# Performance work log

Hardware: AMD Instinct MI355X
Metric: run time of the kernel (lower is better)

## Reference

```python
import jax, jax.numpy as jnp
import numpy as np

B, S, D, H = 4, 4096, 1024, 16
DK = D // H  # 64


def setup_inputs() -> dict:
    key = jax.random.key(0)
    ks = jax.random.split(key, 8)
    scale = 1.0 / np.sqrt(D)
    return {
        "query": jax.random.normal(ks[0], (B, S, D), dtype=jnp.float32),
        "key": jax.random.normal(ks[1], (B, S, D), dtype=jnp.float32),
        "value": jax.random.normal(ks[2], (B, S, D), dtype=jnp.float32),
        "Wq": jax.random.normal(ks[3], (D, D), dtype=jnp.float32) * scale,
        "Wk": jax.random.normal(ks[4], (D, D), dtype=jnp.float32) * scale,
        "Wv": jax.random.normal(ks[5], (D, D), dtype=jnp.float32) * scale,
        "Wo": jax.random.normal(ks[6], (D, D), dtype=jnp.float32) * scale,
        "bo": jnp.zeros((D,), dtype=jnp.float32),
    }


def _phi(x):
    # ELU + 1 feature map
    return jax.nn.elu(x) + 1.0


def _heads(x, W):
    # torch Linear: y = x @ W.T; then [B,S,D] -> [B,H,S,DK]
    y = jnp.einsum("bsd,ed->bse", x, W)
    return y.reshape(x.shape[0], x.shape[1], H, DK).transpose(0, 2, 1, 3)


def reference(query, key, value, Wq, Wk, Wv, Wo, bo):
    Q = _phi(_heads(query, Wq))   # [B,H,Sq,DK]
    K = _phi(_heads(key, Wk))     # [B,H,Sk,DK]
    V = _heads(value, Wv)         # [B,H,Sk,DK]

    KV = jnp.einsum("bhsd,bhse->bhde", K, V)        # [B,H,DK,DK]
    num = jnp.einsum("bhqd,bhde->bhqe", Q, KV)       # [B,H,Sq,DK]
    den = jnp.einsum("bhqd,bhd->bhq", Q, K.sum(axis=2))  # [B,H,Sq]
    out = num / (den[..., None] + 1e-6)

    out = out.transpose(0, 2, 1, 3).reshape(query.shape[0], query.shape[1], D)
    return jnp.einsum("bsd,ed->bse", out, Wo) + bo
```

## Files before the change

kernel.cpp:

```cpp
#include <hip/hip_runtime.h>


typedef unsigned short ushort_t;
typedef __bf16 bf16x8 __attribute__((ext_vector_type(8)));
typedef float f32x4 __attribute__((ext_vector_type(4)));
typedef void gvoid_t __attribute__((address_space(1)));
typedef void svoid_t __attribute__((address_space(3)));

#define BB 4
#define SS 4096
#define DD 1024
#define HH 16
#define DKk 64
#define MM (BB * SS)

__device__ __forceinline__ ushort_t f2bf(float f) {
  unsigned int u = __float_as_uint(f);
  u += 0x7fffu + ((u >> 16) & 1u);
  return (ushort_t)(u >> 16);
}
__device__ __forceinline__ float b2f(ushort_t h) {
  return __uint_as_float(((unsigned int)h) << 16);
}
__device__ __forceinline__ void gld_lds16(const ushort_t* g, ushort_t* l) {
  __builtin_amdgcn_global_load_lds((gvoid_t*)g, (svoid_t*)l, 16, 0, 0);
}
__device__ __forceinline__ bf16x8 ldfrag(const ushort_t* p) {
  return *(const bf16x8*)p;
}

__global__ __launch_bounds__(256) void cast3_kernel(
    const float* __restrict__ q, const float* __restrict__ k, const float* __restrict__ v,
    ushort_t* __restrict__ qd, ushort_t* __restrict__ kd, ushort_t* __restrict__ vd) {
  const int z = blockIdx.y;
  const float* s = (z == 0) ? q : (z == 1) ? k : v;
  ushort_t* d = (z == 0) ? qd : (z == 1) ? kd : vd;
  size_t i = ((size_t)blockIdx.x * 256 + threadIdx.x) * 4;
  float4 f = *(const float4*)(s + i);
  ushort4 o;
  o.x = f2bf(f.x); o.y = f2bf(f.y); o.z = f2bf(f.z); o.w = f2bf(f.w);
  *(ushort4*)(d + i) = o;
}

__global__ __launch_bounds__(256) void cast4_kernel(
    const float* __restrict__ a, const float* __restrict__ b,
    const float* __restrict__ c, const float* __restrict__ e,
    ushort_t* __restrict__ ad, ushort_t* __restrict__ bd,
    ushort_t* __restrict__ cd, ushort_t* __restrict__ ed) {
  const int z = blockIdx.y;
  const float* s = (z == 0) ? a : (z == 1) ? b : (z == 2) ? c : e;
  ushort_t* d = (z == 0) ? ad : (z == 1) ? bd : (z == 2) ? cd : ed;
  size_t i = ((size_t)blockIdx.x * 256 + threadIdx.x) * 4;
  float4 f = *(const float4*)(s + i);
  ushort4 o;
  o.x = f2bf(f.x); o.y = f2bf(f.y); o.z = f2bf(f.z); o.w = f2bf(f.w);
  *(ushort4*)(d + i) = o;
}

__global__ __launch_bounds__(256) void proj_kernel(
    const ushort_t* __restrict__ qa, const ushort_t* __restrict__ ka, const ushort_t* __restrict__ va,
    const ushort_t* __restrict__ wq, const ushort_t* __restrict__ wk, const ushort_t* __restrict__ wv,
    ushort_t* __restrict__ Qp, ushort_t* __restrict__ Kp, ushort_t* __restrict__ Vp) {
  const int z = blockIdx.z;
  const ushort_t* A = (z == 0) ? qa : (z == 1) ? ka : va;
  const ushort_t* Bw = (z == 0) ? wq : (z == 1) ? wk : wv;
  ushort_t* Y = (z == 0) ? Qp : (z == 1) ? Kp : Vp;
  const bool act = (z < 2);

  __shared__ __align__(16) ushort_t Ash[2][128 * 32];
  __shared__ __align__(16) ushort_t Bsh[2][128 * 32];
  const int t = threadIdx.x;
  const int r_ = blockIdx.x, u_ = blockIdx.y;
  const int yb = r_ + 8 * (u_ & 7) + 64 * (u_ >> 6);
  const int xb = (u_ >> 3) & 7;
  const int m0 = yb * 128, n0 = xb * 128;
  const int w = t >> 6, lane = t & 63, q4 = lane >> 4, l16 = lane & 15;
  const int wm = (w >> 1) * 64, wn = (w & 1) * 64;
  const int srow = t >> 2, sch = (t & 3) * 8;

  f32x4 acc[4][4];
  const f32x4 zero = {0.f, 0.f, 0.f, 0.f};
#pragma unroll
  for (int i = 0; i < 4; i++)
#pragma unroll
    for (int j = 0; j < 4; j++) acc[i][j] = zero;

  const ushort_t* ga = A + (size_t)(m0 + srow) * 1024 + sch;
  const ushort_t* gb = Bw + (size_t)(n0 + srow) * 1024 + sch;

  gld_lds16(ga + 0, &Ash[0][t * 8]);
  gld_lds16(ga + 64 * 1024, &Ash[0][(256 + t) * 8]);
  gld_lds16(gb + 0, &Bsh[0][t * 8]);
  gld_lds16(gb + 64 * 1024, &Bsh[0][(256 + t) * 8]);
  __syncthreads();

  int cur = 0;
  for (int k0 = 0; k0 < 1024; k0 += 32, cur ^= 1) {
    if (k0 + 32 < 1024) {
      gld_lds16(ga + (k0 + 32), &Ash[cur ^ 1][t * 8]);
      gld_lds16(ga + (k0 + 32) + 64 * 1024, &Ash[cur ^ 1][(256 + t) * 8]);
      gld_lds16(gb + (k0 + 32), &Bsh[cur ^ 1][t * 8]);
      gld_lds16(gb + (k0 + 32) + 64 * 1024, &Bsh[cur ^ 1][(256 + t) * 8]);
    }
    bf16x8 af[4], bfm[4];
#pragma unroll
    for (int mi = 0; mi < 4; mi++) af[mi] = ldfrag(&Ash[cur][(wm + mi * 16 + l16) * 32 + q4 * 8]);
#pragma unroll
    for (int ni = 0; ni < 4; ni++) bfm[ni] = ldfrag(&Bsh[cur][(wn + ni * 16 + l16) * 32 + q4 * 8]);
#pragma unroll
    for (int mi = 0; mi < 4; mi++)
#pragma unroll
      for (int ni = 0; ni < 4; ni++)
        acc[mi][ni] = __builtin_amdgcn_mfma_f32_16x16x32_bf16(af[mi], bfm[ni], acc[mi][ni], 0, 0, 0);
    __syncthreads();
  }
#pragma unroll
  for (int mi = 0; mi < 4; mi++)
#pragma unroll
    for (int ni = 0; ni < 4; ni++) {
      int col = n0 + wn + ni * 16 + l16;
#pragma unroll
      for (int r = 0; r < 4; r++) {
        int row = m0 + wm + mi * 16 + q4 * 4 + r;
        float vv = acc[mi][ni][r];
        if (act) vv = (vv > 0.f) ? (vv + 1.f) : __expf(vv);
        Y[(size_t)row * 1024 + col] = f2bf(vv);
      }
    }
}

__global__ __launch_bounds__(256) void out_kernel(
    const ushort_t* __restrict__ A, const ushort_t* __restrict__ Bw,
    float* __restrict__ Of, const float* __restrict__ bias) {
  __shared__ __align__(16) ushort_t Ash[2][128 * 32];
  __shared__ __align__(16) ushort_t Bsh[2][128 * 32];
  const int t = threadIdx.x;
  const int r_ = blockIdx.x, u_ = blockIdx.y;
  const int yb = r_ + 8 * (u_ & 7) + 64 * (u_ >> 6);
  const int xb = (u_ >> 3) & 7;
  const int m0 = yb * 128, n0 = xb * 128;
  const int w = t >> 6, lane = t & 63, q4 = lane >> 4, l16 = lane & 15;
  const int wm = (w >> 1) * 64, wn = (w & 1) * 64;
  const int srow = t >> 2, sch = (t & 3) * 8;

  f32x4 acc[4][4];
  const f32x4 zero = {0.f, 0.f, 0.f, 0.f};
#pragma unroll
  for (int i = 0; i < 4; i++)
#pragma unroll
    for (int j = 0; j < 4; j++) acc[i][j] = zero;

  const ushort_t* ga = A + (size_t)(m0 + srow) * 1024 + sch;
  const ushort_t* gb = Bw + (size_t)(n0 + srow) * 1024 + sch;

  gld_lds16(ga + 0, &Ash[0][t * 8]);
  gld_lds16(ga + 64 * 1024, &Ash[0][(256 + t) * 8]);
  gld_lds16(gb + 0, &Bsh[0][t * 8]);
  gld_lds16(gb + 64 * 1024, &Bsh[0][(256 + t) * 8]);
  __syncthreads();

  int cur = 0;
  for (int k0 = 0; k0 < 1024; k0 += 32, cur ^= 1) {
    if (k0 + 32 < 1024) {
      gld_lds16(ga + (k0 + 32), &Ash[cur ^ 1][t * 8]);
      gld_lds16(ga + (k0 + 32) + 64 * 1024, &Ash[cur ^ 1][(256 + t) * 8]);
      gld_lds16(gb + (k0 + 32), &Bsh[cur ^ 1][t * 8]);
      gld_lds16(gb + (k0 + 32) + 64 * 1024, &Bsh[cur ^ 1][(256 + t) * 8]);
    }
    bf16x8 af[4], bfm[4];
#pragma unroll
    for (int mi = 0; mi < 4; mi++) af[mi] = ldfrag(&Ash[cur][(wm + mi * 16 + l16) * 32 + q4 * 8]);
#pragma unroll
    for (int ni = 0; ni < 4; ni++) bfm[ni] = ldfrag(&Bsh[cur][(wn + ni * 16 + l16) * 32 + q4 * 8]);
#pragma unroll
    for (int mi = 0; mi < 4; mi++)
#pragma unroll
      for (int ni = 0; ni < 4; ni++)
        acc[mi][ni] = __builtin_amdgcn_mfma_f32_16x16x32_bf16(af[mi], bfm[ni], acc[mi][ni], 0, 0, 0);
    __syncthreads();
  }
#pragma unroll
  for (int mi = 0; mi < 4; mi++)
#pragma unroll
    for (int ni = 0; ni < 4; ni++) {
      int col = n0 + wn + ni * 16 + l16;
      float bv = bias[col];
#pragma unroll
      for (int r = 0; r < 4; r++) {
        int row = m0 + wm + mi * 16 + q4 * 4 + r;
        Of[(size_t)row * 1024 + col] = acc[mi][ni][r] + bv;
      }
    }
}

__global__ __launch_bounds__(256) void kv_kernel(
    const ushort_t* __restrict__ Kp, const ushort_t* __restrict__ Vp,
    float* __restrict__ KVt, float* __restrict__ Ksum) {
  const int bh = blockIdx.y, b = bh >> 4, h = bh & 15;
  const int schunk = blockIdx.x * 256;
  const int t = threadIdx.x, w = t >> 6, lane = t & 63, q4 = lane >> 4, l16 = lane & 15;
  __shared__ ushort_t Ksh[64 * 66];
  __shared__ ushort_t Vsh[64 * 66];
  __shared__ float red[4][64];

  f32x4 acc[4];
  const f32x4 zero = {0.f, 0.f, 0.f, 0.f};
#pragma unroll
  for (int i = 0; i < 4; i++) acc[i] = zero;
  float ksum = 0.f;

  const int mat = t >> 7, tl = t & 127;
  const ushort_t* src = mat ? Vp : Kp;
  ushort_t* dsh = mat ? Vsh : Ksh;

  for (int tile = 0; tile < 4; tile++) {
    const int s0 = schunk + tile * 64;
#pragma unroll
    for (int i = 0; i < 4; i++) {
      int idx = i * 1024 + tl * 8;
      int r = idx >> 6, c = idx & 63;
      const ushort_t* g = src + (size_t)(b * 4096 + s0 + r) * 1024 + h * 64 + c;
      uint4 u = *(const uint4*)g;
      unsigned int* p = (unsigned int*)&dsh[r * 66 + c];
      p[0] = u.x; p[1] = u.y; p[2] = u.z; p[3] = u.w;
    }
    __syncthreads();
#pragma unroll
    for (int ks = 0; ks < 2; ks++) {
      ushort_t tb[8];
#pragma unroll
      for (int j = 0; j < 8; j++) tb[j] = Ksh[(ks * 32 + q4 * 8 + j) * 66 + w * 16 + l16];
      bf16x8 bfr; __builtin_memcpy(&bfr, tb, 16);
#pragma unroll
      for (int mi = 0; mi < 4; mi++) {
        ushort_t ta[8];
#pragma unroll
        for (int j = 0; j < 8; j++) ta[j] = Vsh[(ks * 32 + q4 * 8 + j) * 66 + mi * 16 + l16];
        bf16x8 afr; __builtin_memcpy(&afr, ta, 16);
        acc[mi] = __builtin_amdgcn_mfma_f32_16x16x32_bf16(afr, bfr, acc[mi], 0, 0, 0);
      }
    }
    {
      int d = t & 63;
#pragma unroll
      for (int r = 0; r < 16; r++) ksum += b2f(Ksh[((t >> 6) * 16 + r) * 66 + d]);
    }
    __syncthreads();
  }
#pragma unroll
  for (int mi = 0; mi < 4; mi++)
#pragma unroll
    for (int r = 0; r < 4; r++) {
      int e = mi * 16 + q4 * 4 + r, d = w * 16 + l16;
      atomicAdd(&KVt[(size_t)bh * 4096 + e * 64 + d], acc[mi][r]);
    }
  red[t >> 6][t & 63] = ksum;
  __syncthreads();
  if (t < 64) atomicAdd(&Ksum[bh * 64 + t], red[0][t] + red[1][t] + red[2][t] + red[3][t]);
}

__global__ __launch_bounds__(256) void num_kernel(
    const ushort_t* __restrict__ Qp, const float* __restrict__ KVt,
    const float* __restrict__ Ksum, ushort_t* __restrict__ Oc) {
  const int bh = blockIdx.y, b = bh >> 4, h = bh & 15;
  const int sblk = blockIdx.x * 256;
  const int t = threadIdx.x, w = t >> 6, lane = t & 63, q4 = lane >> 4, l16 = lane & 15;
  __shared__ __align__(16) ushort_t KVsh[64 * 72];
  __shared__ float Ks_sh[64];
  __shared__ float rden[256];

#pragma unroll
  for (int i = 0; i < 16; i++) {
    int idx = i * 256 + t;
    int e = idx >> 6, d = idx & 63;
    KVsh[e * 72 + d] = f2bf(KVt[(size_t)bh * 4096 + idx]);
  }
  if (t < 64) Ks_sh[t] = Ksum[bh * 64 + t];
  __syncthreads();

  {
    const ushort_t* qrow = Qp + (size_t)(b * 4096 + sblk + t) * 1024 + h * 64;
    float den = 1e-6f;
#pragma unroll
    for (int j = 0; j < 8; j++) {
      bf16x8 qv = ldfrag(qrow + j * 8);
#pragma unroll
      for (int e = 0; e < 8; e++) den += (float)qv[e] * Ks_sh[j * 8 + e];
    }
    rden[t] = 1.f / den;
  }
  __syncthreads();

  f32x4 acc[4][4];
  const f32x4 zero = {0.f, 0.f, 0.f, 0.f};
#pragma unroll
  for (int i = 0; i < 4; i++)
#pragma unroll
    for (int j = 0; j < 4; j++) acc[i][j] = zero;

#pragma unroll
  for (int ks = 0; ks < 2; ks++) {
    bf16x8 af[4], bfr[4];
#pragma unroll
    for (int mi = 0; mi < 4; mi++)
      af[mi] = ldfrag(Qp + (size_t)(b * 4096 + sblk + w * 64 + mi * 16 + l16) * 1024 + h * 64 + ks * 32 + q4 * 8);
#pragma unroll
    for (int ni = 0; ni < 4; ni++)
      bfr[ni] = ldfrag(&KVsh[(ni * 16 + l16) * 72 + ks * 32 + q4 * 8]);
#pragma unroll
    for (int mi = 0; mi < 4; mi++)
#pragma unroll
      for (int ni = 0; ni < 4; ni++)
        acc[mi][ni] = __builtin_amdgcn_mfma_f32_16x16x32_bf16(af[mi], bfr[ni], acc[mi][ni], 0, 0, 0);
  }
#pragma unroll
  for (int mi = 0; mi < 4; mi++)
#pragma unroll
    for (int ni = 0; ni < 4; ni++) {
      int e = ni * 16 + l16;
#pragma unroll
      for (int r = 0; r < 4; r++) {
        int srow = w * 64 + mi * 16 + q4 * 4 + r;
        float vv = acc[mi][ni][r] * rden[srow];
        Oc[(size_t)(b * 4096 + sblk + srow) * 1024 + h * 64 + e] = f2bf(vv);
      }
    }
}

extern "C" void kernel_launch(void* const* d_in, const int* in_sizes, int n_in,
                              void* d_out, int out_size, void* d_ws, size_t ws_size,
                              hipStream_t stream) {
  const float* q  = (const float*)d_in[0];
  const float* k  = (const float*)d_in[1];
  const float* v  = (const float*)d_in[2];
  const float* Wq = (const float*)d_in[3];
  const float* Wk = (const float*)d_in[4];
  const float* Wv = (const float*)d_in[5];
  const float* Wo = (const float*)d_in[6];
  const float* bo = (const float*)d_in[7];

  char* ws = (char*)d_ws;
  const size_t SZ_IN = (size_t)MM * DD * 2;
  ushort_t* qbf = (ushort_t*)(ws);
  ushort_t* kbf = (ushort_t*)(ws + SZ_IN);
  ushort_t* vbf = (ushort_t*)(ws + 2 * SZ_IN);
  ushort_t* wqb = (ushort_t*)(ws + 3 * SZ_IN);
  ushort_t* wkb = wqb + (size_t)1024 * 1024;
  ushort_t* wvb = wkb + (size_t)1024 * 1024;
  ushort_t* wob = wvb + (size_t)1024 * 1024;
  ushort_t* Qp  = (ushort_t*)(ws + 3 * SZ_IN + 4 * (size_t)2097152);
  ushort_t* Kp  = Qp + (size_t)MM * DD;
  ushort_t* Vp  = Kp + (size_t)MM * DD;
  float* KVt    = (float*)((char*)(Vp + (size_t)MM * DD));
  float* KsumP  = KVt + (size_t)64 * 4096;
  ushort_t* Oc  = qbf;
  float* outp   = (float*)d_out;

  hipMemsetAsync(KVt, 0, ((size_t)64 * 4096 + 64 * 64) * sizeof(float), stream);
  cast3_kernel<<<dim3(16384, 3), 256, 0, stream>>>(q, k, v, qbf, kbf, vbf);
  cast4_kernel<<<dim3(1024, 4), 256, 0, stream>>>(Wq, Wk, Wv, Wo, wqb, wkb, wvb, wob);
  proj_kernel<<<dim3(8, 128, 3), 256, 0, stream>>>(qbf, kbf, vbf, wqb, wkb, wvb, Qp, Kp, Vp);
  kv_kernel<<<dim3(16, 64), 256, 0, stream>>>(Kp, Vp, KVt, KsumP);
  num_kernel<<<dim3(16, 64), 256, 0, stream>>>(Qp, KVt, KsumP, Oc);
  out_kernel<<<dim3(8, 128), 256, 0, stream>>>(Oc, wob, outp, bo);
}
```

Measured before the change: 453.7 us.

## Replace 128x128 GEMMs with 256x256 tiled, swizzled, ping-pong scheduled GEMM core

Both the projection and output GEMMs now use a shared 256x256-tile core with 512 threads, BK=64, XOR-swizzled LDS layout, and a staged load schedule with explicit waitcnt, barriers and setprio around MFMA clusters. Blocks are remapped so consecutive blocks land on different XCDs. The larger tiles raise arithmetic intensity and cut global traffic, and the swizzle avoids LDS bank conflicts. In exchange, register and LDS pressure go up, and with 768 and 256 blocks the wave quantization could be worse.

After: 430.0 us. 5.2% less time.

```diff
diff --git a/kernel.cpp b/kernel.cpp
--- a/kernel.cpp
+++ b/kernel.cpp
@@ -13,6 +13,7 @@
 #define HH 16
 #define DKk 64
 #define MM (BB * SS)
+#define NKT 16
 
 __device__ __forceinline__ ushort_t f2bf(float f) {
   unsigned int u = __float_as_uint(f);
@@ -57,140 +58,181 @@
   *(ushort4*)(d + i) = o;
 }
 
-__global__ __launch_bounds__(256) void proj_kernel(
+__device__ __forceinline__ void gemm256_core(
+    const ushort_t* __restrict__ A, const ushort_t* __restrict__ Bw,
+    ushort_t* __restrict__ Ybf, float* __restrict__ Yf,
+    const float* __restrict__ bias, bool act, int m0, int n0) {
+  __shared__ __align__(16) ushort_t As[2][2][8192];
+  __shared__ __align__(16) ushort_t Bs[2][2][8192];
+  const int t = threadIdx.x;
+  const int w = t >> 6, lane = t & 63, q4 = lane >> 4, l16 = lane & 15;
+  const int wr = w >> 2, wc = w & 3;
+  const int srow = t >> 3;
+  const int scol = (((t & 7) ^ (srow & 7)) * 8);
+  const int swz = l16 & 7;
+
+  const ushort_t* gA = A + (size_t)(m0 + srow) * 1024 + scol;
+  const ushort_t* gB = Bw + (size_t)(n0 + srow) * 1024 + scol;
+
+  f32x4 acc[8][4];
+  const f32x4 zero = {0.f, 0.f, 0.f, 0.f};
+#pragma unroll
+  for (int i = 0; i < 8; ++i)
+#pragma unroll
+    for (int j = 0; j < 4; ++j) acc[i][j] = zero;
+
+  auto rdA = [&](int c, int mi, int kk) -> bf16x8 {
+    const int rowh = mi * 16 + l16;
+    const int slot = (kk * 4 + q4) ^ swz;
+    return ldfrag(&As[c][wr][rowh * 64 + slot * 8]);
+  };
+  auto rdB = [&](int c, int ni, int kk) -> bf16x8 {
+    const int rowh = (wc & 1) * 64 + ni * 16 + l16;
+    const int slot = (kk * 4 + q4) ^ swz;
+    return ldfrag(&Bs[c][wc >> 1][rowh * 64 + slot * 8]);
+  };
+  auto stageA = [&](int c, int h, int kt) {
+    const ushort_t* g = gA + (size_t)(h * 128) * 1024 + kt * 64;
+    gld_lds16(g, &As[c][h][t * 8]);
+    gld_lds16(g + 64 * 1024, &As[c][h][4096 + t * 8]);
+  };
+  auto stageB = [&](int c, int h, int kt) {
+    const ushort_t* g = gB + (size_t)(h * 128) * 1024 + kt * 64;
+    gld_lds16(g, &Bs[c][h][t * 8]);
+    gld_lds16(g + 64 * 1024, &Bs[c][h][4096 + t * 8]);
+  };
+
+  stageB(0, 0, 0); stageB(0, 1, 0);
+  stageA(0, 0, 0); stageA(0, 1, 0);
+  stageB(1, 0, 1); stageB(1, 1, 1);
+  asm volatile("s_waitcnt vmcnt(4)" ::: "memory");
+  __builtin_amdgcn_s_barrier();
+
+  bf16x8 aR[4][2], b0[2][2], b1[2][2];
+#pragma unroll 2
+  for (int kt = 0; kt < NKT; ++kt) {
+    const int c = kt & 1;
+#pragma unroll
+    for (int mi = 0; mi < 4; ++mi) { aR[mi][0] = rdA(c, mi, 0); aR[mi][1] = rdA(c, mi, 1); }
+#pragma unroll
+    for (int ni = 0; ni < 2; ++ni) { b0[ni][0] = rdB(c, ni, 0); b0[ni][1] = rdB(c, ni, 1); }
+    if (kt + 1 < NKT) stageA(c ^ 1, 0, kt + 1);
+    __builtin_amdgcn_s_barrier();
+    asm volatile("s_waitcnt lgkmcnt(0)" ::: "memory");
+    __builtin_amdgcn_sched_barrier(0);
+    __builtin_amdgcn_s_setprio(1);
+#pragma unroll
+    for (int mi = 0; mi < 4; ++mi)
+#pragma unroll
+      for (int ni = 0; ni < 2; ++ni) {
+        acc[mi][ni] = __builtin_amdgcn_mfma_f32_16x16x32_bf16(aR[mi][0], b0[ni][0], acc[mi][ni], 0, 0, 0);
+        acc[mi][ni] = __builtin_amdgcn_mfma_f32_16x16x32_bf16(aR[mi][1], b0[ni][1], acc[mi][ni], 0, 0, 0);
+      }
+    __builtin_amdgcn_s_setprio(0);
+    __builtin_amdgcn_s_barrier();
+#pragma unroll
+    for (int ni = 0; ni < 2; ++ni) { b1[ni][0] = rdB(c, ni + 2, 0); b1[ni][1] = rdB(c, ni + 2, 1); }
+    if (kt + 1 < NKT) stageA(c ^ 1, 1, kt + 1);
+    __builtin_amdgcn_s_barrier();
+    asm volatile("s_waitcnt lgkmcnt(0)" ::: "memory");
+    __builtin_amdgcn_sched_barrier(0);
+    __builtin_amdgcn_s_setprio(1);
+#pragma unroll
+    for (int mi = 0; mi < 4; ++mi)
+#pragma unroll
+      for (int ni = 0; ni < 2; ++ni) {
+        acc[mi][ni + 2] = __builtin_amdgcn_mfma_f32_16x16x32_bf16(aR[mi][0], b1[ni][0], acc[mi][ni + 2], 0, 0, 0);
+        acc[mi][ni + 2] = __builtin_amdgcn_mfma_f32_16x16x32_bf16(aR[mi][1], b1[ni][1], acc[mi][ni + 2], 0, 0, 0);
+      }
+    __builtin_amdgcn_s_setprio(0);
+    __builtin_amdgcn_s_barrier();
+#pragma unroll
+    for (int mi = 0; mi < 4; ++mi) { aR[mi][0] = rdA(c, mi + 4, 0); aR[mi][1] = rdA(c, mi + 4, 1); }
+    if (kt + 2 < NKT) stageB(c, 0, kt + 2);
+    __builtin_amdgcn_s_barrier();
+    asm volatile("s_waitcnt lgkmcnt(0)" ::: "memory");
+    __builtin_amdgcn_sched_barrier(0);
+    __builtin_amdgcn_s_setprio(1);
+#pragma unroll
+    for (int mi = 0; mi < 4; ++mi)
+#pragma unroll
+      for (int ni = 0; ni < 2; ++ni) {
+        acc[mi + 4][ni] = __builtin_amdgcn_mfma_f32_16x16x32_bf16(aR[mi][0], b0[ni][0], acc[mi + 4][ni], 0, 0, 0);
+        acc[mi + 4][ni] = __builtin_amdgcn_mfma_f32_16x16x32_bf16(aR[mi][1], b0[ni][1], acc[mi + 4][ni], 0, 0, 0);
+      }
+    __builtin_amdgcn_s_setprio(0);
+    __builtin_amdgcn_s_barrier();
+    if (kt + 2 < NKT) stageB(c, 1, kt + 2);
+    __builtin_amdgcn_s_barrier();
+    __builtin_amdgcn_s_setprio(1);
+#pragma unroll
+    for (int mi = 0; mi < 4; ++mi)
+#pragma unroll
+      for (int ni = 0; ni < 2; ++ni) {
+        acc[mi + 4][ni + 2] = __builtin_amdgcn_mfma_f32_16x16x32_bf16(aR[mi][0], b1[ni][0], acc[mi + 4][ni + 2], 0, 0, 0);
+        acc[mi + 4][ni + 2] = __builtin_amdgcn_mfma_f32_16x16x32_bf16(aR[mi][1], b1[ni][1], acc[mi + 4][ni + 2], 0, 0, 0);
+      }
+    __builtin_amdgcn_s_setprio(0);
+    if (kt < NKT - 2) {
+      asm volatile("s_waitcnt vmcnt(4)" ::: "memory");
+    } else if (kt == NKT - 2) {
+      asm volatile("s_waitcnt vmcnt(0)" ::: "memory");
+    }
+    __builtin_amdgcn_s_barrier();
+  }
+
+  if (Yf) {
+#pragma unroll
+    for (int mi = 0; mi < 8; ++mi)
+#pragma unroll
+      for (int ni = 0; ni < 4; ++ni) {
+        const int col = n0 + wc * 64 + ni * 16 + l16;
+        const float bv = bias[col];
+#pragma unroll
+        for (int r = 0; r < 4; ++r) {
+          const int row = m0 + wr * 128 + mi * 16 + q4 * 4 + r;
+          Yf[(size_t)row * 1024 + col] = acc[mi][ni][r] + bv;
+        }
+      }
+  } else {
+#pragma unroll
+    for (int mi = 0; mi < 8; ++mi)
+#pragma unroll
+      for (int ni = 0; ni < 4; ++ni) {
+        const int col = n0 + wc * 64 + ni * 16 + l16;
+#pragma unroll
+        for (int r = 0; r < 4; ++r) {
+          const int row = m0 + wr * 128 + mi * 16 + q4 * 4 + r;
+          float vv = acc[mi][ni][r];
+          if (act) vv = (vv > 0.f) ? (vv + 1.f) : __expf(vv);
+          Ybf[(size_t)row * 1024 + col] = f2bf(vv);
+        }
+      }
+  }
+}
+
+__global__ __launch_bounds__(512, 2) void proj256_kernel(
     const ushort_t* __restrict__ qa, const ushort_t* __restrict__ ka, const ushort_t* __restrict__ va,
     const ushort_t* __restrict__ wq, const ushort_t* __restrict__ wk, const ushort_t* __restrict__ wv,
     ushort_t* __restrict__ Qp, ushort_t* __restrict__ Kp, ushort_t* __restrict__ Vp) {
-  const int z = blockIdx.z;
+  const int raw = blockIdx.x;
+  const int logical = (raw & 7) * 96 + (raw >> 3);
+  const int z = logical >> 8;
+  const int rem = logical & 255;
+  const int m0 = (rem >> 2) * 256, n0 = (rem & 3) * 256;
   const ushort_t* A = (z == 0) ? qa : (z == 1) ? ka : va;
   const ushort_t* Bw = (z == 0) ? wq : (z == 1) ? wk : wv;
   ushort_t* Y = (z == 0) ? Qp : (z == 1) ? Kp : Vp;
-  const bool act = (z < 2);
-
-  __shared__ __align__(16) ushort_t Ash[2][128 * 32];
-  __shared__ __align__(16) ushort_t Bsh[2][128 * 32];
-  const int t = threadIdx.x;
-  const int r_ = blockIdx.x, u_ = blockIdx.y;
-  const int yb = r_ + 8 * (u_ & 7) + 64 * (u_ >> 6);
-  const int xb = (u_ >> 3) & 7;
-  const int m0 = yb * 128, n0 = xb * 128;
-  const int w = t >> 6, lane = t & 63, q4 = lane >> 4, l16 = lane & 15;
-  const int wm = (w >> 1) * 64, wn = (w & 1) * 64;
-  const int srow = t >> 2, sch = (t & 3) * 8;
-
-  f32x4 acc[4][4];
-  const f32x4 zero = {0.f, 0.f, 0.f, 0.f};
-#pragma unroll
-  for (int i = 0; i < 4; i++)
-#pragma unroll
-    for (int j = 0; j < 4; j++) acc[i][j] = zero;
-
-  const ushort_t* ga = A + (size_t)(m0 + srow) * 1024 + sch;
-  const ushort_t* gb = Bw + (size_t)(n0 + srow) * 1024 + sch;
-
-  gld_lds16(ga + 0, &Ash[0][t * 8]);
-  gld_lds16(ga + 64 * 1024, &Ash[0][(256 + t) * 8]);
-  gld_lds16(gb + 0, &Bsh[0][t * 8]);
-  gld_lds16(gb + 64 * 1024, &Bsh[0][(256 + t) * 8]);
-  __syncthreads();
-
-  int cur = 0;
-  for (int k0 = 0; k0 < 1024; k0 += 32, cur ^= 1) {
-    if (k0 + 32 < 1024) {
-      gld_lds16(ga + (k0 + 32), &Ash[cur ^ 1][t * 8]);
-      gld_lds16(ga + (k0 + 32) + 64 * 1024, &Ash[cur ^ 1][(256 + t) * 8]);
-      gld_lds16(gb + (k0 + 32), &Bsh[cur ^ 1][t * 8]);
-      gld_lds16(gb + (k0 + 32) + 64 * 1024, &Bsh[cur ^ 1][(256 + t) * 8]);
-    }
-    bf16x8 af[4], bfm[4];
-#pragma unroll
-    for (int mi = 0; mi < 4; mi++) af[mi] = ldfrag(&Ash[cur][(wm + mi * 16 + l16) * 32 + q4 * 8]);
-#pragma unroll
-    for (int ni = 0; ni < 4; ni++) bfm[ni] = ldfrag(&Bsh[cur][(wn + ni * 16 + l16) * 32 + q4 * 8]);
-#pragma unroll
-    for (int mi = 0; mi < 4; mi++)
-#pragma unroll
-      for (int ni = 0; ni < 4; ni++)
-        acc[mi][ni] = __builtin_amdgcn_mfma_f32_16x16x32_bf16(af[mi], bfm[ni], acc[mi][ni], 0, 0, 0);
-    __syncthreads();
-  }
-#pragma unroll
-  for (int mi = 0; mi < 4; mi++)
-#pragma unroll
-    for (int ni = 0; ni < 4; ni++) {
-      int col = n0 + wn + ni * 16 + l16;
-#pragma unroll
-      for (int r = 0; r < 4; r++) {
-        int row = m0 + wm + mi * 16 + q4 * 4 + r;
-        float vv = acc[mi][ni][r];
-        if (act) vv = (vv > 0.f) ? (vv + 1.f) : __expf(vv);
-        Y[(size_t)row * 1024 + col] = f2bf(vv);
-      }
-    }
-}
-
-__global__ __launch_bounds__(256) void out_kernel(
+  gemm256_core(A, Bw, Y, nullptr, nullptr, z < 2, m0, n0);
+}
+
+__global__ __launch_bounds__(512, 2) void out256_kernel(
     const ushort_t* __restrict__ A, const ushort_t* __restrict__ Bw,
     float* __restrict__ Of, const float* __restrict__ bias) {
-  __shared__ __align__(16) ushort_t Ash[2][128 * 32];
-  __shared__ __align__(16) ushort_t Bsh[2][128 * 32];
-  const int t = threadIdx.x;
-  const int r_ = blockIdx.x, u_ = blockIdx.y;
-  const int yb = r_ + 8 * (u_ & 7) + 64 * (u_ >> 6);
-  const int xb = (u_ >> 3) & 7;
-  const int m0 = yb * 128, n0 = xb * 128;
-  const int w = t >> 6, lane = t & 63, q4 = lane >> 4, l16 = lane & 15;
-  const int wm = (w >> 1) * 64, wn = (w & 1) * 64;
-  const int srow = t >> 2, sch = (t & 3) * 8;
-
-  f32x4 acc[4][4];
-  const f32x4 zero = {0.f, 0.f, 0.f, 0.f};
-#pragma unroll
-  for (int i = 0; i < 4; i++)
-#pragma unroll
-    for (int j = 0; j < 4; j++) acc[i][j] = zero;
-
-  const ushort_t* ga = A + (size_t)(m0 + srow) * 1024 + sch;
-  const ushort_t* gb = Bw + (size_t)(n0 + srow) * 1024 + sch;
-
-  gld_lds16(ga + 0, &Ash[0][t * 8]);
-  gld_lds16(ga + 64 * 1024, &Ash[0][(256 + t) * 8]);
-  gld_lds16(gb + 0, &Bsh[0][t * 8]);
-  gld_lds16(gb + 64 * 1024, &Bsh[0][(256 + t) * 8]);
-  __syncthreads();
-
-  int cur = 0;
-  for (int k0 = 0; k0 < 1024; k0 += 32, cur ^= 1) {
-    if (k0 + 32 < 1024) {
-      gld_lds16(ga + (k0 + 32), &Ash[cur ^ 1][t * 8]);
-      gld_lds16(ga + (k0 + 32) + 64 * 1024, &Ash[cur ^ 1][(256 + t) * 8]);
-      gld_lds16(gb + (k0 + 32), &Bsh[cur ^ 1][t * 8]);
-      gld_lds16(gb + (k0 + 32) + 64 * 1024, &Bsh[cur ^ 1][(256 + t) * 8]);
-    }
-    bf16x8 af[4], bfm[4];
-#pragma unroll
-    for (int mi = 0; mi < 4; mi++) af[mi] = ldfrag(&Ash[cur][(wm + mi * 16 + l16) * 32 + q4 * 8]);
-#pragma unroll
-    for (int ni = 0; ni < 4; ni++) bfm[ni] = ldfrag(&Bsh[cur][(wn + ni * 16 + l16) * 32 + q4 * 8]);
-#pragma unroll
-    for (int mi = 0; mi < 4; mi++)
-#pragma unroll
-      for (int ni = 0; ni < 4; ni++)
-        acc[mi][ni] = __builtin_amdgcn_mfma_f32_16x16x32_bf16(af[mi], bfm[ni], acc[mi][ni], 0, 0, 0);
-    __syncthreads();
-  }
-#pragma unroll
-  for (int mi = 0; mi < 4; mi++)
-#pragma unroll
-    for (int ni = 0; ni < 4; ni++) {
-      int col = n0 + wn + ni * 16 + l16;
-      float bv = bias[col];
-#pragma unroll
-      for (int r = 0; r < 4; r++) {
-        int row = m0 + wm + mi * 16 + q4 * 4 + r;
-        Of[(size_t)row * 1024 + col] = acc[mi][ni][r] + bv;
-      }
-    }
+  const int raw = blockIdx.x;
+  const int logical = (raw & 7) * 32 + (raw >> 3);
+  const int m0 = (logical >> 2) * 256, n0 = (logical & 3) * 256;
+  gemm256_core(A, Bw, nullptr, Of, bias, false, m0, n0);
 }
 
 __global__ __launch_bounds__(256) void kv_kernel(
@@ -359,8 +401,8 @@
   hipMemsetAsync(KVt, 0, ((size_t)64 * 4096 + 64 * 64) * sizeof(float), stream);
   cast3_kernel<<<dim3(16384, 3), 256, 0, stream>>>(q, k, v, qbf, kbf, vbf);
   cast4_kernel<<<dim3(1024, 4), 256, 0, stream>>>(Wq, Wk, Wv, Wo, wqb, wkb, wvb, wob);
-  proj_kernel<<<dim3(8, 128, 3), 256, 0, stream>>>(qbf, kbf, vbf, wqb, wkb, wvb, Qp, Kp, Vp);
+  proj256_kernel<<<dim3(768), 512, 0, stream>>>(qbf, kbf, vbf, wqb, wkb, wvb, Qp, Kp, Vp);
   kv_kernel<<<dim3(16, 64), 256, 0, stream>>>(Kp, Vp, KVt, KsumP);
   num_kernel<<<dim3(16, 64), 256, 0, stream>>>(Qp, KVt, KsumP, Oc);
-  out_kernel<<<dim3(8, 128), 256, 0, stream>>>(Oc, wob, outp, bo);
-}
+  out256_kernel<<<dim3(256), 512, 0, stream>>>(Oc, wob, outp, bo);
+}
```
